# Optimization experiments

Measured on AMD Instinct MI355X. Metric: run time of the kernel, lower is better.

Reference implementation:

```python
import jax, jax.numpy as jnp
import numpy as np

N_NODES = 100000


def gcn_conv(x, edge_index, W, b):
    # PyG GCNConv: h = D^{-1/2} (A + I) D^{-1/2} (x @ W) + b
    N = x.shape[0]
    h = x @ W  # [N, C_out]
    loops = jnp.arange(N, dtype=edge_index.dtype)
    src = jnp.concatenate([edge_index[0], loops])
    dst = jnp.concatenate([edge_index[1], loops])
    deg = jax.ops.segment_sum(jnp.ones_like(dst, dtype=h.dtype), dst, num_segments=N)
    inv_sqrt = jnp.where(deg > 0, jax.lax.rsqrt(deg), 0.0)
    norm = inv_sqrt[src] * inv_sqrt[dst]              # [E+N]
    msg = h[src] * norm[:, None]                      # gather + scale
    out = jax.ops.segment_sum(msg, dst, num_segments=N)  # scatter-add
    return out + b


def setup_inputs() -> dict:
    key = jax.random.key(0)
    ks = jax.random.split(key, 6)
    x = jax.random.normal(ks[0], (N_NODES, 4), dtype=jnp.float32)
    edge_index = jax.random.randint(ks[1], (2, 3200000), 0, N_NODES, dtype=jnp.int32)
    edge_label_index = jax.random.randint(ks[2], (2, 200000), 0, N_NODES, dtype=jnp.int32)
    W1 = jax.random.normal(ks[3], (4, 128), dtype=jnp.float32) * (1.0 / np.sqrt(4))
    b1 = jnp.zeros((128,), dtype=jnp.float32)
    W2 = jax.random.normal(ks[4], (128, 64), dtype=jnp.float32) * (1.0 / np.sqrt(128))
    b2 = jnp.zeros((64,), dtype=jnp.float32)
    return {"x": x, "edge_index": edge_index, "edge_label_index": edge_label_index,
            "W1": W1, "b1": b1, "W2": W2, "b2": b2}


def reference(x, edge_index, edge_label_index, W1, b1, W2, b2):
    h = jax.nn.relu(gcn_conv(x, edge_index, W1, b1))
    z = gcn_conv(h, edge_index, W2, b2)               # encode -> [N, 64]
    # decode: dot product per labeled edge -> [E_lbl]
    logits = jnp.sum(z[edge_label_index[0]] * z[edge_label_index[1]], axis=-1)
    return logits
```

## Files before the change

kernel.cpp:

```cpp
#include <hip/hip_runtime.h>

#define N_NODES 100000
#define N_EDGES 3200000
#define N_LBL   200000
#define C1 128
#define C2 64

#define BSH   7
#define NPB   128
#define NBKT  ((N_NODES + NPB - 1) / NPB)
#define NCB   500
#define PPT   512
#define CHUNK (N_EDGES / NCB)
#define CAP   4992

#define RSTRIDE 132

__device__ __forceinline__ float4 f4add(float4 a, float4 b) {
    return make_float4(a.x + b.x, a.y + b.y, a.z + b.z, a.w + b.w);
}
__device__ __forceinline__ unsigned short f2bf(float f) {
    unsigned int u = __float_as_uint(f);
    u += 0x7fff + ((u >> 16) & 1);
    return (unsigned short)(u >> 16);
}
__device__ __forceinline__ float bflo(unsigned int u) {
    return __uint_as_float(u << 16);
}
__device__ __forceinline__ float bfhi(unsigned int u) {
    return __uint_as_float(u & 0xffff0000u);
}

__global__ __launch_bounds__(PPT) void pair_place_kernel(const int* __restrict__ ei,
        int* __restrict__ gcursor, unsigned int* __restrict__ pairs) {
    __shared__ int hist[NBKT];
    __shared__ int cur[NBKT];
    int tid = threadIdx.x;
    for (int i = tid; i < NBKT; i += PPT) hist[i] = 0;
    __syncthreads();
    int base = blockIdx.x * CHUNK;
    unsigned int pk[13]; int bkt[13]; int rnk[13];
    #pragma unroll
    for (int k = 0; k < 13; ++k) {
        if (k < 12 || tid < CHUNK - 12 * PPT) {
            int e = base + k * PPT + tid;
            int s = ei[e], d = ei[N_EDGES + e];
            int b = d >> BSH;
            bkt[k] = b;
            pk[k] = ((unsigned int)(d & (NPB - 1)) << 17) | (unsigned int)s;
            rnk[k] = atomicAdd(&hist[b], 1);
        }
    }
    __syncthreads();
    for (int i = tid; i < NBKT; i += PPT) {
        int h = hist[i];
        cur[i] = h ? (i * CAP + atomicAdd(&gcursor[i], h)) : 0;
    }
    __syncthreads();
    #pragma unroll
    for (int k = 0; k < 13; ++k) {
        if (k < 12 || tid < CHUNK - 12 * PPT) {
            int pos = cur[bkt[k]] + rnk[k];
            pos = min(pos, NBKT * CAP - 1);
            pairs[pos] = pk[k];
        }
    }
}

__global__ __launch_bounds__(512) void bucket_finish_kernel(
        const unsigned int* __restrict__ pairs, const int* __restrict__ gcursor,
        const float4* __restrict__ x, int* __restrict__ offs, int* __restrict__ ends,
        float* __restrict__ inv, float4* __restrict__ xs, int* __restrict__ srcs) {
    __shared__ int deg[NPB];
    __shared__ int nstart[NPB];
    __shared__ int wsum2[2];
    int tid = threadIdx.x;
    int b = blockIdx.x;
    int nbase = b << BSH;
    int eb = b * CAP;
    int ee = eb + min(gcursor[b], CAP);
    if (tid < NPB) deg[tid] = 0;
    __syncthreads();
    unsigned int pk[10]; int rnk[10];
    #pragma unroll
    for (int k = 0; k < 10; ++k) {
        int j = eb + k * 512 + tid;
        if (j < ee) {
            unsigned int p = pairs[j];
            pk[k] = p;
            rnk[k] = atomicAdd(&deg[p >> 17], 1);
        }
    }
    __syncthreads();
    int v = 0, incl = 0;
    if (tid < NPB) {
        int lane = tid & 63;
        v = deg[tid];
        incl = v;
        #pragma unroll
        for (int off = 1; off < 64; off <<= 1) {
            int t = __shfl_up(incl, off);
            if (lane >= off) incl += t;
        }
        if (lane == 63) wsum2[tid >> 6] = incl;
    }
    __syncthreads();
    if (tid < NPB) {
        int excl = incl - v + ((tid >= 64) ? wsum2[0] : 0);
        int start = eb + excl;
        nstart[tid] = start;
        int n = nbase + tid;
        if (n < N_NODES) {
            offs[n] = start;
            ends[n] = start + v;
            float iv = rsqrtf((float)(v + 1));
            inv[n] = iv;
            float4 xv = x[n];
            xv.x *= iv; xv.y *= iv; xv.z *= iv; xv.w *= iv;
            xs[n] = xv;
        }
    }
    __syncthreads();
    #pragma unroll
    for (int k = 0; k < 10; ++k) {
        int j = eb + k * 512 + tid;
        if (j < ee) {
            unsigned int p = pk[k];
            srcs[nstart[p >> 17] + rnk[k]] = (int)(p & 0x1FFFFu);
        }
    }
}

__global__ __launch_bounds__(256) void agg1_gemm12_kernel(
        const float4* __restrict__ xs, const int* __restrict__ offs,
        const int* __restrict__ ends, const int* __restrict__ srcs,
        const float* __restrict__ inv, const float* __restrict__ W1,
        const float* __restrict__ b1, const float* __restrict__ W2,
        unsigned short* __restrict__ hs2b) {
    __shared__ float w1s[4 * C1];
    __shared__ float bs[C1];
    __shared__ unsigned int w2b[C1 * C2 / 2];
    __shared__ float rows[64 * RSTRIDE];
    int tid = threadIdx.x;
    int base = blockIdx.x * 64;
    w1s[tid] = W1[tid];
    w1s[tid + 256] = W1[tid + 256];
    if (tid < C1) bs[tid] = b1[tid];
    {
        const float2* w2f = (const float2*)W2;
        for (int i = tid; i < C1 * C2 / 2; i += 256) {
            float2 v = w2f[i];
            w2b[i] = (unsigned int)f2bf(v.x) | ((unsigned int)f2bf(v.y) << 16);
        }
    }
    int nd = tid >> 2, g = tid & 3;
    int n = base + nd;
    float4 acc0 = make_float4(0.f, 0.f, 0.f, 0.f);
    {
        if (n < N_NODES) {
            if (g == 0) acc0 = xs[n];
            int e = ends[n];
            for (int j = offs[n] + g; j < e; j += 4)
                acc0 = f4add(acc0, xs[srcs[j]]);
        }
        acc0.x += __shfl_xor(acc0.x, 1); acc0.y += __shfl_xor(acc0.y, 1);
        acc0.z += __shfl_xor(acc0.z, 1); acc0.w += __shfl_xor(acc0.w, 1);
        acc0.x += __shfl_xor(acc0.x, 2); acc0.y += __shfl_xor(acc0.y, 2);
        acc0.z += __shfl_xor(acc0.z, 2); acc0.w += __shfl_xor(acc0.w, 2);
    }
    __syncthreads();
    {
        float s = (n < N_NODES) ? inv[n] : 0.f;
        float4 t = acc0;
        t.x *= s; t.y *= s; t.z *= s; t.w *= s;
        #pragma unroll 8
        for (int cc = 0; cc < 32; ++cc) {
            int c = g + 4 * cc;
            float h = t.x * w1s[c] + t.y * w1s[C1 + c] + t.z * w1s[2 * C1 + c]
                    + t.w * w1s[3 * C1 + c] + bs[c];
            rows[nd * RSTRIDE + c] = fmaxf(h, 0.f);
        }
    }
    __syncthreads();
    int q = tid & 15;
    int ng = tid >> 4;
    float4 acc[4];
    #pragma unroll
    for (int j = 0; j < 4; ++j) acc[j] = make_float4(0.f, 0.f, 0.f, 0.f);
    #pragma unroll 4
    for (int k = 0; k < C1; ++k) {
        uint2 wp = ((const uint2*)w2b)[k * 16 + q];
        float wx = bflo(wp.x), wy = bfhi(wp.x);
        float wz = bflo(wp.y), ww = bfhi(wp.y);
        #pragma unroll
        for (int j = 0; j < 4; ++j) {
            float r = rows[(ng * 4 + j) * RSTRIDE + k];
            acc[j].x += r * wx; acc[j].y += r * wy;
            acc[j].z += r * wz; acc[j].w += r * ww;
        }
    }
    #pragma unroll
    for (int j = 0; j < 4; ++j) {
        int m = base + ng * 4 + j;
        if (m < N_NODES) {
            float s = inv[m];
            ushort4 o;
            o.x = f2bf(acc[j].x * s); o.y = f2bf(acc[j].y * s);
            o.z = f2bf(acc[j].z * s); o.w = f2bf(acc[j].w * s);
            *((ushort4*)(hs2b + (size_t)m * C2) + q) = o;
        }
    }
}

__global__ void agg2_kernel(const unsigned short* __restrict__ hs2b,
                            const int* __restrict__ offs, const int* __restrict__ ends,
                            const int* __restrict__ srcs, const float* __restrict__ inv,
                            const float4* __restrict__ b2,
                            unsigned short* __restrict__ zb) {
    int gid = blockIdx.x * blockDim.x + threadIdx.x;
    int n = gid >> 6;
    if (n >= N_NODES) return;
    int lane = gid & 63;
    int q = lane & 7;
    int g = lane >> 3;
    float acc[8] = {0.f, 0.f, 0.f, 0.f, 0.f, 0.f, 0.f, 0.f};
    if (g == 0) {
        uint4 v = *((const uint4*)(hs2b + (size_t)n * C2) + q);
        acc[0] += bflo(v.x); acc[1] += bfhi(v.x);
        acc[2] += bflo(v.y); acc[3] += bfhi(v.y);
        acc[4] += bflo(v.z); acc[5] += bfhi(v.z);
        acc[6] += bflo(v.w); acc[7] += bfhi(v.w);
    }
    int e = ends[n];
    int j = offs[n] + g;
    for (; j + 8 < e; j += 16) {
        int s0 = srcs[j];
        int s1 = srcs[j + 8];
        uint4 v0 = *((const uint4*)(hs2b + (size_t)s0 * C2) + q);
        uint4 v1 = *((const uint4*)(hs2b + (size_t)s1 * C2) + q);
        acc[0] += bflo(v0.x); acc[1] += bfhi(v0.x);
        acc[2] += bflo(v0.y); acc[3] += bfhi(v0.y);
        acc[4] += bflo(v0.z); acc[5] += bfhi(v0.z);
        acc[6] += bflo(v0.w); acc[7] += bfhi(v0.w);
        acc[0] += bflo(v1.x); acc[1] += bfhi(v1.x);
        acc[2] += bflo(v1.y); acc[3] += bfhi(v1.y);
        acc[4] += bflo(v1.z); acc[5] += bfhi(v1.z);
        acc[6] += bflo(v1.w); acc[7] += bfhi(v1.w);
    }
    if (j < e) {
        int s0 = srcs[j];
        uint4 v0 = *((const uint4*)(hs2b + (size_t)s0 * C2) + q);
        acc[0] += bflo(v0.x); acc[1] += bfhi(v0.x);
        acc[2] += bflo(v0.y); acc[3] += bfhi(v0.y);
        acc[4] += bflo(v0.z); acc[5] += bfhi(v0.z);
        acc[6] += bflo(v0.w); acc[7] += bfhi(v0.w);
    }
    #pragma unroll
    for (int k = 0; k < 8; ++k) {
        acc[k] += __shfl_xor(acc[k], 8);
        acc[k] += __shfl_xor(acc[k], 16);
        acc[k] += __shfl_xor(acc[k], 32);
    }
    if (g == 0) {
        float s = inv[n];
        float4 b0 = b2[q * 2], b1v = b2[q * 2 + 1];
        float o0 = acc[0] * s + b0.x,  o1 = acc[1] * s + b0.y;
        float o2 = acc[2] * s + b0.z,  o3 = acc[3] * s + b0.w;
        float o4 = acc[4] * s + b1v.x, o5 = acc[5] * s + b1v.y;
        float o6 = acc[6] * s + b1v.z, o7 = acc[7] * s + b1v.w;
        uint4 w;
        w.x = (unsigned int)f2bf(o0) | ((unsigned int)f2bf(o1) << 16);
        w.y = (unsigned int)f2bf(o2) | ((unsigned int)f2bf(o3) << 16);
        w.z = (unsigned int)f2bf(o4) | ((unsigned int)f2bf(o5) << 16);
        w.w = (unsigned int)f2bf(o6) | ((unsigned int)f2bf(o7) << 16);
        ((uint4*)(zb + (size_t)n * C2))[q] = w;
    }
}

__global__ void decode_kernel(const int* __restrict__ eli,
                              const unsigned short* __restrict__ zb,
                              float* __restrict__ out) {
    int gid = blockIdx.x * blockDim.x + threadIdx.x;
    int e = gid >> 3;
    if (e >= N_LBL) return;
    int q = gid & 7;
    int a = eli[e], b = eli[N_LBL + e];
    uint4 va = ((const uint4*)zb)[(size_t)a * 8 + q];
    uint4 vb = ((const uint4*)zb)[(size_t)b * 8 + q];
    float p = bflo(va.x) * bflo(vb.x) + bfhi(va.x) * bfhi(vb.x)
            + bflo(va.y) * bflo(vb.y) + bfhi(va.y) * bfhi(vb.y)
            + bflo(va.z) * bflo(vb.z) + bfhi(va.z) * bfhi(vb.z)
            + bflo(va.w) * bflo(vb.w) + bfhi(va.w) * bfhi(vb.w);
    p += __shfl_xor(p, 4);
    p += __shfl_xor(p, 2);
    p += __shfl_xor(p, 1);
    if (q == 0) out[e] = p;
}

extern "C" void kernel_launch(void* const* d_in, const int* in_sizes, int n_in,
                              void* d_out, int out_size, void* d_ws, size_t ws_size,
                              hipStream_t stream) {
    const float* x  = (const float*)d_in[0];
    const int*   ei = (const int*)d_in[1];
    const int*  eli = (const int*)d_in[2];
    const float* W1 = (const float*)d_in[3];
    const float* b1 = (const float*)d_in[4];
    const float* W2 = (const float*)d_in[5];
    const float* b2 = (const float*)d_in[6];
    float* out = (float*)d_out;

    char* p = (char*)d_ws;
    int*   gcursor = (int*)p;   p += 1024 * 4;
    int*   offs    = (int*)p;   p += (size_t)N_NODES * 4;
    int*   ends    = (int*)p;   p += (size_t)N_NODES * 4;
    float* inv     = (float*)p; p += (size_t)N_NODES * 4;
    unsigned int* pairs = (unsigned int*)p; p += (size_t)NBKT * CAP * 4;
    int*   srcs    = (int*)p;   p += (size_t)NBKT * CAP * 4;
    float* xs      = (float*)p; p += (size_t)N_NODES * 16;
    unsigned short* hs2b = (unsigned short*)p; p += (size_t)N_NODES * C2 * 2;
    unsigned short* zb   = (unsigned short*)p; p += (size_t)N_NODES * C2 * 2;

    hipMemsetAsync(gcursor, 0, NBKT * 4, stream);
    pair_place_kernel<<<NCB, PPT, 0, stream>>>(ei, gcursor, pairs);
    bucket_finish_kernel<<<NBKT, 512, 0, stream>>>(pairs, gcursor, (const float4*)x,
                                                   offs, ends, inv, (float4*)xs, srcs);
    agg1_gemm12_kernel<<<(N_NODES + 63) / 64, 256, 0, stream>>>(
        (const float4*)xs, offs, ends, srcs, inv, W1, b1, W2, hs2b);
    agg2_kernel<<<((size_t)N_NODES * 64 + 255) / 256, 256, 0, stream>>>(
        hs2b, offs, ends, srcs, inv, (const float4*)b2, zb);
    decode_kernel<<<((size_t)N_LBL * 8 + 255) / 256, 256, 0, stream>>>(eli, zb, out);
}
```

Before: 254.1 us.

## Split agg2 gather into column-slice passes for better cache locality

```diff
diff --git a/kernel.cpp b/kernel.cpp
--- a/kernel.cpp
+++ b/kernel.cpp
@@ -15,6 +15,8 @@
 #define CAP   4992
 
 #define RSTRIDE 132
+
+typedef unsigned int uint4n __attribute__((ext_vector_type(4)));
 
 __device__ __forceinline__ float4 f4add(float4 a, float4 b) {
     return make_float4(a.x + b.x, a.y + b.y, a.z + b.z, a.w + b.w);
@@ -217,27 +219,31 @@
                             const int* __restrict__ srcs, const float* __restrict__ inv,
                             const float4* __restrict__ b2,
                             unsigned short* __restrict__ zb) {
-    int gid = blockIdx.x * blockDim.x + threadIdx.x;
-    int n = gid >> 6;
-    if (n >= N_NODES) return;
-    int lane = gid & 63;
-    int q = lane & 7;
-    int g = lane >> 3;
+    int slot = blockIdx.x & 7;
+    int pass = slot >> 1;
+    int nblk = (blockIdx.x >> 3) * 2 + (slot & 1);
+    int tid  = threadIdx.x;
+    int n = nblk * 16 + (tid >> 6) * 4 + ((tid >> 4) & 3);
+    int r = tid & 15;
+    int q = r & 1;
+    int g = r >> 1;
+    int c = pass * 2 + q;
+    const uint4* tab = (const uint4*)hs2b;
     float acc[8] = {0.f, 0.f, 0.f, 0.f, 0.f, 0.f, 0.f, 0.f};
     if (g == 0) {
-        uint4 v = *((const uint4*)(hs2b + (size_t)n * C2) + q);
+        uint4 v = tab[(size_t)n * 8 + c];
         acc[0] += bflo(v.x); acc[1] += bfhi(v.x);
         acc[2] += bflo(v.y); acc[3] += bfhi(v.y);
         acc[4] += bflo(v.z); acc[5] += bfhi(v.z);
         acc[6] += bflo(v.w); acc[7] += bfhi(v.w);
     }
-    int e = ends[n];
-    int j = offs[n] + g;
+    int e = __builtin_nontemporal_load(&ends[n]);
+    int j = __builtin_nontemporal_load(&offs[n]) + g;
     for (; j + 8 < e; j += 16) {
-        int s0 = srcs[j];
-        int s1 = srcs[j + 8];
-        uint4 v0 = *((const uint4*)(hs2b + (size_t)s0 * C2) + q);
-        uint4 v1 = *((const uint4*)(hs2b + (size_t)s1 * C2) + q);
+        int s0 = __builtin_nontemporal_load(&srcs[j]);
+        int s1 = __builtin_nontemporal_load(&srcs[j + 8]);
+        uint4 v0 = tab[(size_t)s0 * 8 + c];
+        uint4 v1 = tab[(size_t)s1 * 8 + c];
         acc[0] += bflo(v0.x); acc[1] += bfhi(v0.x);
         acc[2] += bflo(v0.y); acc[3] += bfhi(v0.y);
         acc[4] += bflo(v0.z); acc[5] += bfhi(v0.z);
@@ -248,8 +254,8 @@
         acc[6] += bflo(v1.w); acc[7] += bfhi(v1.w);
     }
     if (j < e) {
-        int s0 = srcs[j];
-        uint4 v0 = *((const uint4*)(hs2b + (size_t)s0 * C2) + q);
+        int s0 = __builtin_nontemporal_load(&srcs[j]);
+        uint4 v0 = tab[(size_t)s0 * 8 + c];
         acc[0] += bflo(v0.x); acc[1] += bfhi(v0.x);
         acc[2] += bflo(v0.y); acc[3] += bfhi(v0.y);
         acc[4] += bflo(v0.z); acc[5] += bfhi(v0.z);
@@ -257,23 +263,23 @@
     }
     #pragma unroll
     for (int k = 0; k < 8; ++k) {
+        acc[k] += __shfl_xor(acc[k], 2);
+        acc[k] += __shfl_xor(acc[k], 4);
         acc[k] += __shfl_xor(acc[k], 8);
-        acc[k] += __shfl_xor(acc[k], 16);
-        acc[k] += __shfl_xor(acc[k], 32);
     }
     if (g == 0) {
-        float s = inv[n];
-        float4 b0 = b2[q * 2], b1v = b2[q * 2 + 1];
+        float s = __builtin_nontemporal_load(&inv[n]);
+        float4 b0 = b2[c * 2], b1v = b2[c * 2 + 1];
         float o0 = acc[0] * s + b0.x,  o1 = acc[1] * s + b0.y;
         float o2 = acc[2] * s + b0.z,  o3 = acc[3] * s + b0.w;
         float o4 = acc[4] * s + b1v.x, o5 = acc[5] * s + b1v.y;
         float o6 = acc[6] * s + b1v.z, o7 = acc[7] * s + b1v.w;
-        uint4 w;
+        uint4n w;
         w.x = (unsigned int)f2bf(o0) | ((unsigned int)f2bf(o1) << 16);
         w.y = (unsigned int)f2bf(o2) | ((unsigned int)f2bf(o3) << 16);
         w.z = (unsigned int)f2bf(o4) | ((unsigned int)f2bf(o5) << 16);
         w.w = (unsigned int)f2bf(o6) | ((unsigned int)f2bf(o7) << 16);
-        ((uint4*)(zb + (size_t)n * C2))[q] = w;
+        __builtin_nontemporal_store(w, (uint4n*)zb + (size_t)n * 8 + c);
     }
 }
 
@@ -320,13 +326,13 @@
     unsigned short* hs2b = (unsigned short*)p; p += (size_t)N_NODES * C2 * 2;
     unsigned short* zb   = (unsigned short*)p; p += (size_t)N_NODES * C2 * 2;
 
-    hipMemsetAsync(gcursor, 0, NBKT * 4, stream);
+    (void)hipMemsetAsync(gcursor, 0, NBKT * 4, stream);
     pair_place_kernel<<<NCB, PPT, 0, stream>>>(ei, gcursor, pairs);
     bucket_finish_kernel<<<NBKT, 512, 0, stream>>>(pairs, gcursor, (const float4*)x,
                                                    offs, ends, inv, (float4*)xs, srcs);
     agg1_gemm12_kernel<<<(N_NODES + 63) / 64, 256, 0, stream>>>(
         (const float4*)xs, offs, ends, srcs, inv, W1, b1, W2, hs2b);
-    agg2_kernel<<<((size_t)N_NODES * 64 + 255) / 256, 256, 0, stream>>>(
+    agg2_kernel<<<(N_NODES / 32) * 8, 256, 0, stream>>>(
         hs2b, offs, ends, srcs, inv, (const float4*)b2, zb);
     decode_kernel<<<((size_t)N_LBL * 8 + 255) / 256, 256, 0, stream>>>(eli, zb, out);
 }
```

Result: slower. 373.9 us (+47.2%).

## Split layer-2 features into channel-half by source-half tables for cache-local gathers

Applied to the files above, without the earlier changes.

```diff
diff --git a/kernel.cpp b/kernel.cpp
--- a/kernel.cpp
+++ b/kernel.cpp
@@ -1,6 +1,7 @@
 #include <hip/hip_runtime.h>
 
 #define N_NODES 100000
+#define N_HALF  50000
 #define N_EDGES 3200000
 #define N_LBL   200000
 #define C1 128
@@ -12,7 +13,7 @@
 #define NCB   500
 #define PPT   512
 #define CHUNK (N_EDGES / NCB)
-#define CAP   4992
+#define CAP   4864
 
 #define RSTRIDE 132
 
@@ -29,6 +30,12 @@
 }
 __device__ __forceinline__ float bfhi(unsigned int u) {
     return __uint_as_float(u & 0xffff0000u);
+}
+__device__ __forceinline__ void acc16(float* acc, uint4 v) {
+    acc[0] += bflo(v.x); acc[1] += bfhi(v.x);
+    acc[2] += bflo(v.y); acc[3] += bfhi(v.y);
+    acc[4] += bflo(v.z); acc[5] += bfhi(v.z);
+    acc[6] += bflo(v.w); acc[7] += bfhi(v.w);
 }
 
 __global__ __launch_bounds__(PPT) void pair_place_kernel(const int* __restrict__ ei,
@@ -69,17 +76,18 @@
 
 __global__ __launch_bounds__(512) void bucket_finish_kernel(
         const unsigned int* __restrict__ pairs, const int* __restrict__ gcursor,
-        const float4* __restrict__ x, int* __restrict__ offs, int* __restrict__ ends,
-        float* __restrict__ inv, float4* __restrict__ xs, int* __restrict__ srcs) {
-    __shared__ int deg[NPB];
-    __shared__ int nstart[NPB];
-    __shared__ int wsum2[2];
+        const float4* __restrict__ x, int* __restrict__ offs, int* __restrict__ mids,
+        int* __restrict__ ends, float* __restrict__ inv, float4* __restrict__ xs,
+        int* __restrict__ srcs) {
+    __shared__ int deg2[NPB * 2];
+    __shared__ int nst2[NPB * 2];
+    __shared__ int wsum4[4];
     int tid = threadIdx.x;
     int b = blockIdx.x;
     int nbase = b << BSH;
     int eb = b * CAP;
     int ee = eb + min(gcursor[b], CAP);
-    if (tid < NPB) deg[tid] = 0;
+    if (tid < NPB * 2) deg2[tid] = 0;
     __syncthreads();
     unsigned int pk[10]; int rnk[10];
     #pragma unroll
@@ -88,32 +96,40 @@
         if (j < ee) {
             unsigned int p = pairs[j];
             pk[k] = p;
-            rnk[k] = atomicAdd(&deg[p >> 17], 1);
+            int idx = (int)((p >> 17) & 127u) * 2 + ((p & 0x1FFFFu) >= (unsigned)N_HALF);
+            rnk[k] = atomicAdd(&deg2[idx], 1);
         }
     }
     __syncthreads();
     int v = 0, incl = 0;
-    if (tid < NPB) {
+    if (tid < NPB * 2) {
         int lane = tid & 63;
-        v = deg[tid];
+        v = deg2[tid];
         incl = v;
         #pragma unroll
         for (int off = 1; off < 64; off <<= 1) {
             int t = __shfl_up(incl, off);
             if (lane >= off) incl += t;
         }
-        if (lane == 63) wsum2[tid >> 6] = incl;
+        if (lane == 63) wsum4[tid >> 6] = incl;
+    }
+    __syncthreads();
+    if (tid < NPB * 2) {
+        int w = tid >> 6;
+        int add = (w > 0 ? wsum4[0] : 0) + (w > 1 ? wsum4[1] : 0) + (w > 2 ? wsum4[2] : 0);
+        nst2[tid] = eb + incl - v + add;
     }
     __syncthreads();
     if (tid < NPB) {
-        int excl = incl - v + ((tid >= 64) ? wsum2[0] : 0);
-        int start = eb + excl;
-        nstart[tid] = start;
         int n = nbase + tid;
         if (n < N_NODES) {
-            offs[n] = start;
-            ends[n] = start + v;
-            float iv = rsqrtf((float)(v + 1));
+            int s0 = nst2[2 * tid];
+            int s1 = nst2[2 * tid + 1];
+            int d1 = deg2[2 * tid + 1];
+            offs[n] = s0;
+            mids[n] = s1;
+            ends[n] = s1 + d1;
+            float iv = rsqrtf((float)((s1 - s0) + d1 + 1));
             inv[n] = iv;
             float4 xv = x[n];
             xv.x *= iv; xv.y *= iv; xv.z *= iv; xv.w *= iv;
@@ -126,7 +142,9 @@
         int j = eb + k * 512 + tid;
         if (j < ee) {
             unsigned int p = pk[k];
-            srcs[nstart[p >> 17] + rnk[k]] = (int)(p & 0x1FFFFu);
+            int src = (int)(p & 0x1FFFFu);
+            int idx = (int)((p >> 17) & 127u) * 2 + (src >= N_HALF);
+            srcs[nst2[idx] + rnk[k]] = src;
         }
     }
 }
@@ -136,7 +154,7 @@
         const int* __restrict__ ends, const int* __restrict__ srcs,
         const float* __restrict__ inv, const float* __restrict__ W1,
         const float* __restrict__ b1, const float* __restrict__ W2,
-        unsigned short* __restrict__ hs2b) {
+        unsigned short* __restrict__ hs2q) {
     __shared__ float w1s[4 * C1];
     __shared__ float bs[C1];
     __shared__ unsigned int w2b[C1 * C2 / 2];
@@ -207,63 +225,69 @@
             ushort4 o;
             o.x = f2bf(acc[j].x * s); o.y = f2bf(acc[j].y * s);
             o.z = f2bf(acc[j].z * s); o.w = f2bf(acc[j].w * s);
-            *((ushort4*)(hs2b + (size_t)m * C2) + q) = o;
-        }
-    }
-}
-
-__global__ void agg2_kernel(const unsigned short* __restrict__ hs2b,
-                            const int* __restrict__ offs, const int* __restrict__ ends,
-                            const int* __restrict__ srcs, const float* __restrict__ inv,
-                            const float4* __restrict__ b2,
+            int hh = q >> 3;
+            int sh = (m >= N_HALF);
+            int local = m - sh * N_HALF;
+            *(ushort4*)(hs2q + ((size_t)(hh * 2 + sh) * N_HALF + local) * 32
+                        + (q & 7) * 4) = o;
+        }
+    }
+}
+
+__global__ __launch_bounds__(256) void agg2_kernel(const unsigned short* __restrict__ hs2q,
+                            const int* __restrict__ offs, const int* __restrict__ mids,
+                            const int* __restrict__ ends, const int* __restrict__ srcs,
+                            const float* __restrict__ inv, const float4* __restrict__ b2,
                             unsigned short* __restrict__ zb) {
-    int gid = blockIdx.x * blockDim.x + threadIdx.x;
-    int n = gid >> 6;
-    if (n >= N_NODES) return;
-    int lane = gid & 63;
-    int q = lane & 7;
-    int g = lane >> 3;
+    int slot = blockIdx.x & 7;
+    int h = slot >> 2;
+    int nblk = (blockIdx.x >> 3) * 4 + (slot & 3);
+    int tid = threadIdx.x;
+    int lane = tid & 63;
+    int q = lane & 3;
+    int g = (lane >> 2) & 7;
+    int n = nblk * 8 + (tid >> 6) * 2 + (lane >> 5);
     float acc[8] = {0.f, 0.f, 0.f, 0.f, 0.f, 0.f, 0.f, 0.f};
-    if (g == 0) {
-        uint4 v = *((const uint4*)(hs2b + (size_t)n * C2) + q);
-        acc[0] += bflo(v.x); acc[1] += bfhi(v.x);
-        acc[2] += bflo(v.y); acc[3] += bfhi(v.y);
-        acc[4] += bflo(v.z); acc[5] += bfhi(v.z);
-        acc[6] += bflo(v.w); acc[7] += bfhi(v.w);
-    }
-    int e = ends[n];
-    int j = offs[n] + g;
-    for (; j + 8 < e; j += 16) {
-        int s0 = srcs[j];
-        int s1 = srcs[j + 8];
-        uint4 v0 = *((const uint4*)(hs2b + (size_t)s0 * C2) + q);
-        uint4 v1 = *((const uint4*)(hs2b + (size_t)s1 * C2) + q);
-        acc[0] += bflo(v0.x); acc[1] += bfhi(v0.x);
-        acc[2] += bflo(v0.y); acc[3] += bfhi(v0.y);
-        acc[4] += bflo(v0.z); acc[5] += bfhi(v0.z);
-        acc[6] += bflo(v0.w); acc[7] += bfhi(v0.w);
-        acc[0] += bflo(v1.x); acc[1] += bfhi(v1.x);
-        acc[2] += bflo(v1.y); acc[3] += bfhi(v1.y);
-        acc[4] += bflo(v1.z); acc[5] += bfhi(v1.z);
-        acc[6] += bflo(v1.w); acc[7] += bfhi(v1.w);
-    }
-    if (j < e) {
-        int s0 = srcs[j];
-        uint4 v0 = *((const uint4*)(hs2b + (size_t)s0 * C2) + q);
-        acc[0] += bflo(v0.x); acc[1] += bfhi(v0.x);
-        acc[2] += bflo(v0.y); acc[3] += bfhi(v0.y);
-        acc[4] += bflo(v0.z); acc[5] += bfhi(v0.z);
-        acc[6] += bflo(v0.w); acc[7] += bfhi(v0.w);
+    {
+        int sh = (n >= N_HALF);
+        int local = n - sh * N_HALF;
+        if (g == 0) {
+            uint4 v = *((const uint4*)(hs2q + (size_t)(h * 2 + sh) * N_HALF * 32)
+                        + (size_t)local * 4 + q);
+            acc16(acc, v);
+        }
+    }
+    int j0 = offs[n], j1 = mids[n], j2 = ends[n];
+    for (int s = 0; s < 2; ++s) {
+        const uint4* tab = (const uint4*)(hs2q + (size_t)(h * 2 + s) * N_HALF * 32);
+        int jb = s ? j1 : j0;
+        int je = s ? j2 : j1;
+        int rebase = s * N_HALF;
+        int j = jb + g;
+        for (; j + 8 < je; j += 16) {
+            int s0 = srcs[j] - rebase;
+            int s1 = srcs[j + 8] - rebase;
+            uint4 v0 = tab[(size_t)s0 * 4 + q];
+            uint4 v1 = tab[(size_t)s1 * 4 + q];
+            acc16(acc, v0);
+            acc16(acc, v1);
+        }
+        if (j < je) {
+            int s0 = srcs[j] - rebase;
+            uint4 v0 = tab[(size_t)s0 * 4 + q];
+            acc16(acc, v0);
+        }
     }
     #pragma unroll
     for (int k = 0; k < 8; ++k) {
+        acc[k] += __shfl_xor(acc[k], 4);
         acc[k] += __shfl_xor(acc[k], 8);
         acc[k] += __shfl_xor(acc[k], 16);
-        acc[k] += __shfl_xor(acc[k], 32);
     }
     if (g == 0) {
+        int c = h * 4 + q;
         float s = inv[n];
-        float4 b0 = b2[q * 2], b1v = b2[q * 2 + 1];
+        float4 b0 = b2[c * 2], b1v = b2[c * 2 + 1];
         float o0 = acc[0] * s + b0.x,  o1 = acc[1] * s + b0.y;
         float o2 = acc[2] * s + b0.z,  o3 = acc[3] * s + b0.w;
         float o4 = acc[4] * s + b1v.x, o5 = acc[5] * s + b1v.y;
@@ -273,7 +297,7 @@
         w.y = (unsigned int)f2bf(o2) | ((unsigned int)f2bf(o3) << 16);
         w.z = (unsigned int)f2bf(o4) | ((unsigned int)f2bf(o5) << 16);
         w.w = (unsigned int)f2bf(o6) | ((unsigned int)f2bf(o7) << 16);
-        ((uint4*)(zb + (size_t)n * C2))[q] = w;
+        ((uint4*)zb)[(size_t)n * 8 + c] = w;
     }
 }
 
@@ -312,21 +336,22 @@
     char* p = (char*)d_ws;
     int*   gcursor = (int*)p;   p += 1024 * 4;
     int*   offs    = (int*)p;   p += (size_t)N_NODES * 4;
+    int*   mids    = (int*)p;   p += (size_t)N_NODES * 4;
     int*   ends    = (int*)p;   p += (size_t)N_NODES * 4;
     float* inv     = (float*)p; p += (size_t)N_NODES * 4;
     unsigned int* pairs = (unsigned int*)p; p += (size_t)NBKT * CAP * 4;
     int*   srcs    = (int*)p;   p += (size_t)NBKT * CAP * 4;
     float* xs      = (float*)p; p += (size_t)N_NODES * 16;
-    unsigned short* hs2b = (unsigned short*)p; p += (size_t)N_NODES * C2 * 2;
+    unsigned short* hs2q = (unsigned short*)p; p += (size_t)N_NODES * C2 * 2;
     unsigned short* zb   = (unsigned short*)p; p += (size_t)N_NODES * C2 * 2;
 
-    hipMemsetAsync(gcursor, 0, NBKT * 4, stream);
+    (void)hipMemsetAsync(gcursor, 0, NBKT * 4, stream);
     pair_place_kernel<<<NCB, PPT, 0, stream>>>(ei, gcursor, pairs);
     bucket_finish_kernel<<<NBKT, 512, 0, stream>>>(pairs, gcursor, (const float4*)x,
-                                                   offs, ends, inv, (float4*)xs, srcs);
+                                                   offs, mids, ends, inv, (float4*)xs, srcs);
     agg1_gemm12_kernel<<<(N_NODES + 63) / 64, 256, 0, stream>>>(
-        (const float4*)xs, offs, ends, srcs, inv, W1, b1, W2, hs2b);
-    agg2_kernel<<<((size_t)N_NODES * 64 + 255) / 256, 256, 0, stream>>>(
-        hs2b, offs, ends, srcs, inv, (const float4*)b2, zb);
+        (const float4*)xs, offs, ends, srcs, inv, W1, b1, W2, hs2q);
+    agg2_kernel<<<N_NODES / 4, 256, 0, stream>>>(
+        hs2q, offs, mids, ends, srcs, inv, (const float4*)b2, zb);
     decode_kernel<<<((size_t)N_LBL * 8 + 255) / 256, 256, 0, stream>>>(eli, zb, out);
 }
```

After: 266.0 us. 1.05x slower.

## Split layer-2 feature table into two channel halves for cache-resident gathers

Applied to the files above, without the earlier changes.

```diff
diff --git a/kernel.cpp b/kernel.cpp
--- a/kernel.cpp
+++ b/kernel.cpp
@@ -29,6 +29,12 @@
 }
 __device__ __forceinline__ float bfhi(unsigned int u) {
     return __uint_as_float(u & 0xffff0000u);
+}
+__device__ __forceinline__ void acc16(float* acc, uint4 v) {
+    acc[0] += bflo(v.x); acc[1] += bfhi(v.x);
+    acc[2] += bflo(v.y); acc[3] += bfhi(v.y);
+    acc[4] += bflo(v.z); acc[5] += bfhi(v.z);
+    acc[6] += bflo(v.w); acc[7] += bfhi(v.w);
 }
 
 __global__ __launch_bounds__(PPT) void pair_place_kernel(const int* __restrict__ ei,
@@ -136,7 +142,7 @@
         const int* __restrict__ ends, const int* __restrict__ srcs,
         const float* __restrict__ inv, const float* __restrict__ W1,
         const float* __restrict__ b1, const float* __restrict__ W2,
-        unsigned short* __restrict__ hs2b) {
+        unsigned short* __restrict__ hs2h) {
     __shared__ float w1s[4 * C1];
     __shared__ float bs[C1];
     __shared__ unsigned int w2b[C1 * C2 / 2];
@@ -207,63 +213,51 @@
             ushort4 o;
             o.x = f2bf(acc[j].x * s); o.y = f2bf(acc[j].y * s);
             o.z = f2bf(acc[j].z * s); o.w = f2bf(acc[j].w * s);
-            *((ushort4*)(hs2b + (size_t)m * C2) + q) = o;
-        }
-    }
-}
-
-__global__ void agg2_kernel(const unsigned short* __restrict__ hs2b,
+            *(ushort4*)(hs2h + ((size_t)(q >> 3) * N_NODES + m) * 32
+                        + (q & 7) * 4) = o;
+        }
+    }
+}
+
+__global__ __launch_bounds__(256) void agg2h_kernel(const unsigned short* __restrict__ tabh,
                             const int* __restrict__ offs, const int* __restrict__ ends,
                             const int* __restrict__ srcs, const float* __restrict__ inv,
                             const float4* __restrict__ b2,
-                            unsigned short* __restrict__ zb) {
+                            unsigned short* __restrict__ zb, int h) {
     int gid = blockIdx.x * blockDim.x + threadIdx.x;
-    int n = gid >> 6;
+    int n = gid >> 5;
     if (n >= N_NODES) return;
-    int lane = gid & 63;
-    int q = lane & 7;
-    int g = lane >> 3;
+    int sub = gid & 31;
+    int q = sub & 3;
+    int g = sub >> 2;
+    const uint4* tab = (const uint4*)tabh;
     float acc[8] = {0.f, 0.f, 0.f, 0.f, 0.f, 0.f, 0.f, 0.f};
     if (g == 0) {
-        uint4 v = *((const uint4*)(hs2b + (size_t)n * C2) + q);
-        acc[0] += bflo(v.x); acc[1] += bfhi(v.x);
-        acc[2] += bflo(v.y); acc[3] += bfhi(v.y);
-        acc[4] += bflo(v.z); acc[5] += bfhi(v.z);
-        acc[6] += bflo(v.w); acc[7] += bfhi(v.w);
+        acc16(acc, tab[(size_t)n * 4 + q]);
     }
     int e = ends[n];
     int j = offs[n] + g;
     for (; j + 8 < e; j += 16) {
         int s0 = srcs[j];
         int s1 = srcs[j + 8];
-        uint4 v0 = *((const uint4*)(hs2b + (size_t)s0 * C2) + q);
-        uint4 v1 = *((const uint4*)(hs2b + (size_t)s1 * C2) + q);
-        acc[0] += bflo(v0.x); acc[1] += bfhi(v0.x);
-        acc[2] += bflo(v0.y); acc[3] += bfhi(v0.y);
-        acc[4] += bflo(v0.z); acc[5] += bfhi(v0.z);
-        acc[6] += bflo(v0.w); acc[7] += bfhi(v0.w);
-        acc[0] += bflo(v1.x); acc[1] += bfhi(v1.x);
-        acc[2] += bflo(v1.y); acc[3] += bfhi(v1.y);
-        acc[4] += bflo(v1.z); acc[5] += bfhi(v1.z);
-        acc[6] += bflo(v1.w); acc[7] += bfhi(v1.w);
+        uint4 v0 = tab[(size_t)s0 * 4 + q];
+        uint4 v1 = tab[(size_t)s1 * 4 + q];
+        acc16(acc, v0);
+        acc16(acc, v1);
     }
     if (j < e) {
-        int s0 = srcs[j];
-        uint4 v0 = *((const uint4*)(hs2b + (size_t)s0 * C2) + q);
-        acc[0] += bflo(v0.x); acc[1] += bfhi(v0.x);
-        acc[2] += bflo(v0.y); acc[3] += bfhi(v0.y);
-        acc[4] += bflo(v0.z); acc[5] += bfhi(v0.z);
-        acc[6] += bflo(v0.w); acc[7] += bfhi(v0.w);
+        acc16(acc, tab[(size_t)srcs[j] * 4 + q]);
     }
     #pragma unroll
     for (int k = 0; k < 8; ++k) {
+        acc[k] += __shfl_xor(acc[k], 4);
         acc[k] += __shfl_xor(acc[k], 8);
         acc[k] += __shfl_xor(acc[k], 16);
-        acc[k] += __shfl_xor(acc[k], 32);
     }
     if (g == 0) {
+        int c = h * 4 + q;
         float s = inv[n];
-        float4 b0 = b2[q * 2], b1v = b2[q * 2 + 1];
+        float4 b0 = b2[c * 2], b1v = b2[c * 2 + 1];
         float o0 = acc[0] * s + b0.x,  o1 = acc[1] * s + b0.y;
         float o2 = acc[2] * s + b0.z,  o3 = acc[3] * s + b0.w;
         float o4 = acc[4] * s + b1v.x, o5 = acc[5] * s + b1v.y;
@@ -273,7 +267,7 @@
         w.y = (unsigned int)f2bf(o2) | ((unsigned int)f2bf(o3) << 16);
         w.z = (unsigned int)f2bf(o4) | ((unsigned int)f2bf(o5) << 16);
         w.w = (unsigned int)f2bf(o6) | ((unsigned int)f2bf(o7) << 16);
-        ((uint4*)(zb + (size_t)n * C2))[q] = w;
+        ((uint4*)zb)[(size_t)n * 8 + c] = w;
     }
 }
 
@@ -317,16 +311,18 @@
     unsigned int* pairs = (unsigned int*)p; p += (size_t)NBKT * CAP * 4;
     int*   srcs    = (int*)p;   p += (size_t)NBKT * CAP * 4;
     float* xs      = (float*)p; p += (size_t)N_NODES * 16;
-    unsigned short* hs2b = (unsigned short*)p; p += (size_t)N_NODES * C2 * 2;
+    unsigned short* hs2h = (unsigned short*)p; p += (size_t)N_NODES * C2 * 2;
     unsigned short* zb   = (unsigned short*)p; p += (size_t)N_NODES * C2 * 2;
 
-    hipMemsetAsync(gcursor, 0, NBKT * 4, stream);
+    (void)hipMemsetAsync(gcursor, 0, NBKT * 4, stream);
     pair_place_kernel<<<NCB, PPT, 0, stream>>>(ei, gcursor, pairs);
     bucket_finish_kernel<<<NBKT, 512, 0, stream>>>(pairs, gcursor, (const float4*)x,
                                                    offs, ends, inv, (float4*)xs, srcs);
     agg1_gemm12_kernel<<<(N_NODES + 63) / 64, 256, 0, stream>>>(
-        (const float4*)xs, offs, ends, srcs, inv, W1, b1, W2, hs2b);
-    agg2_kernel<<<((size_t)N_NODES * 64 + 255) / 256, 256, 0, stream>>>(
-        hs2b, offs, ends, srcs, inv, (const float4*)b2, zb);
+        (const float4*)xs, offs, ends, srcs, inv, W1, b1, W2, hs2h);
+    agg2h_kernel<<<((size_t)N_NODES * 32 + 255) / 256, 256, 0, stream>>>(
+        hs2h, offs, ends, srcs, inv, (const float4*)b2, zb, 0);
+    agg2h_kernel<<<((size_t)N_NODES * 32 + 255) / 256, 256, 0, stream>>>(
+        hs2h + (size_t)N_NODES * 32, offs, ends, srcs, inv, (const float4*)b2, zb, 1);
     decode_kernel<<<((size_t)N_LBL * 8 + 255) / 256, 256, 0, stream>>>(eli, zb, out);
 }
```

Measured after the change: 266.2 us. 4.8% more time.
